# Kernel tuning notes

Measured on AMD Instinct MI355X. Metric: run time of the kernel, lower is better.

## Reference

```python
import jax, jax.numpy as jnp
from jax import lax
import numpy as np

DN = ('NCHW', 'OIHW', 'NCHW')
EPS = 1e-5


def conv3(x, w, b=None):
    # 3x3 conv, stride 1, padding 1 (SAME)
    y = lax.conv_general_dilated(x, w, (1, 1), 'SAME', dimension_numbers=DN)
    return y if b is None else y + b[None, :, None, None]


def bn_relu(x, gamma, beta):
    # training-mode BatchNorm2d (batch statistics over N,H,W) + ReLU
    m = jnp.mean(x, axis=(0, 2, 3), keepdims=True)
    v = jnp.var(x, axis=(0, 2, 3), keepdims=True)
    y = (x - m) * lax.rsqrt(v + EPS)
    y = y * gamma[None, :, None, None] + beta[None, :, None, None]
    return jax.nn.relu(y)


def _w(key, o, i):
    # torch init: normal(0, sqrt(2/(k*k*out)))
    std = np.sqrt(2.0 / (3 * 3 * o))
    return jax.random.normal(key, (o, i, 3, 3), dtype=jnp.float32) * std


def setup_inputs() -> dict:
    key = jax.random.key(0)
    ks = jax.random.split(key, 16)
    C = 256
    Ch = C // 2
    B, H, W = 4, 160, 160
    d = {}
    d['fpn_fea'] = jax.random.normal(ks[0], (B, C, H, W), dtype=jnp.float32)
    # sc_smooth_layer: conv(C->C)+BN+ReLU, conv(C->C/2)+BN+ReLU (no conv bias)
    d['w_sc1'] = _w(ks[1], C, C); d['g_sc1'] = jnp.ones((C,)); d['b_sc1'] = jnp.zeros((C,))
    d['w_sc2'] = _w(ks[2], Ch, C); d['g_sc2'] = jnp.ones((Ch,)); d['b_sc2'] = jnp.zeros((Ch,))
    # shrink / centroid heads: plain conv(C/2 -> 1) with bias
    d['w_shrink'] = _w(ks[3], 1, Ch); d['bias_shrink'] = jnp.zeros((1,))
    d['w_cent'] = _w(ks[4], 1, Ch); d['bias_cent'] = jnp.zeros((1,))
    # param_head
    d['w_p1'] = _w(ks[5], C, C); d['g_p1'] = jnp.ones((C,)); d['b_p1'] = jnp.zeros((C,))
    d['w_p2'] = _w(ks[6], Ch, C); d['g_p2'] = jnp.ones((Ch,)); d['b_p2'] = jnp.zeros((Ch,))
    d['w_p3'] = _w(ks[7], 2, Ch); d['bias_p3'] = jnp.zeros((2,))
    # shift_head
    d['w_s1'] = _w(ks[8], C, C); d['g_s1'] = jnp.ones((C,)); d['b_s1'] = jnp.zeros((C,))
    d['w_s2'] = _w(ks[9], Ch, C); d['g_s2'] = jnp.ones((Ch,)); d['b_s2'] = jnp.zeros((Ch,))
    d['w_s3'] = _w(ks[10], 8, Ch); d['bias_s3'] = jnp.zeros((8,))
    return d


def reference(fpn_fea, w_sc1, g_sc1, b_sc1, w_sc2, g_sc2, b_sc2,
              w_shrink, bias_shrink, w_cent, bias_cent,
              w_p1, g_p1, b_p1, w_p2, g_p2, b_p2, w_p3, bias_p3,
              w_s1, g_s1, b_s1, w_s2, g_s2, b_s2, w_s3, bias_s3):
    smooth = bn_relu(conv3(fpn_fea, w_sc1), g_sc1, b_sc1)
    smooth = bn_relu(conv3(smooth, w_sc2), g_sc2, b_sc2)
    shrink = conv3(smooth, w_shrink, bias_shrink)      # [B,1,H,W]
    centroid = conv3(smooth, w_cent, bias_cent)        # [B,1,H,W]
    p = bn_relu(conv3(fpn_fea, w_p1), g_p1, b_p1)
    p = bn_relu(conv3(p, w_p2), g_p2, b_p2)
    param = conv3(p, w_p3, bias_p3)                    # [B,2,H,W]
    s = bn_relu(conv3(fpn_fea, w_s1), g_s1, b_s1)
    s = bn_relu(conv3(s, w_s2), g_s2, b_s2)
    shift = conv3(s, w_s3, bias_s3)                    # [B,8,H,W]
    return (shrink, centroid, param, shift)
```

## Files before the change

kernel.cpp:

```cpp
#include <hip/hip_runtime.h>

typedef short bf16x8 __attribute__((ext_vector_type(8)));
typedef float f32x4 __attribute__((ext_vector_type(4)));

__device__ __forceinline__ float bf2f(unsigned short u) {
    union { unsigned int i; float f; } c; c.i = ((unsigned int)u) << 16; return c.f;
}
__device__ __forceinline__ unsigned short f2bf(float f) {
    union { float f; unsigned int i; } c; c.f = f;
    unsigned int u = c.i;
    u += 0x7fffu + ((u >> 16) & 1u);
    return (unsigned short)(u >> 16);
}

__device__ __forceinline__ void gload_lds16(const unsigned short* g, unsigned short* l) {
    __builtin_amdgcn_global_load_lds(
        (const __attribute__((address_space(1))) void*)g,
        (__attribute__((address_space(3))) void*)l, 16, 0, 0);
}


__device__ __forceinline__ void zero_border_one(unsigned short* buf, int C, int idx) {
    int CV = C >> 3;
    int cv = idx % CV; int t = idx / CV;
    int p = t % 644;   int n = t / 644;
    int h, w;
    if (p < 162)      { h = 0;   w = p; }
    else if (p < 324) { h = 161; w = p - 162; }
    else { int q = p - 324; h = 1 + (q >> 1); w = (q & 1) ? 161 : 0; }
    uint4 z = make_uint4(0u, 0u, 0u, 0u);
    *(uint4*)(buf + ((size_t)((n * 162 + h) * 162) + w) * C + cv * 8) = z;
}

__device__ __forceinline__ void do_zero(unsigned short* xpad,
                                        unsigned short* buf1, size_t s1,
                                        unsigned short* buf2, size_t s2, int nbr, int idx) {
    if (idx < 82432) { zero_border_one(xpad, 256, idx); return; }
    idx -= 82432;
    int nb1 = nbr * 82432;
    if (idx < nb1) { zero_border_one(buf1 + (size_t)(idx / 82432) * s1, 256, idx % 82432); return; }
    idx -= nb1;
    int nb2 = nbr * 41216;
    if (idx < nb2) { zero_border_one(buf2 + (size_t)(idx / 41216) * s2, 128, idx % 41216); }
}

__device__ __forceinline__ void do_transpose(const float* __restrict__ x,
                                             unsigned short* __restrict__ xpad, int idx) {
    int w = idx % 160; int t = idx / 160;
    int cv = t % 32;   t /= 32;
    int h = t % 160;   int n = t / 160;
    const float* src = x + (((size_t)(n * 256 + cv * 8) * 160 + h) * 160 + w);
    unsigned short us[8];
#pragma unroll
    for (int k = 0; k < 8; ++k) us[k] = f2bf(src[(size_t)k * 25600]);
    uint4 o;
    o.x = (unsigned int)us[0] | ((unsigned int)us[1] << 16);
    o.y = (unsigned int)us[2] | ((unsigned int)us[3] << 16);
    o.z = (unsigned int)us[4] | ((unsigned int)us[5] << 16);
    o.w = (unsigned int)us[6] | ((unsigned int)us[7] << 16);
    *(uint4*)(xpad + ((size_t)((n * 162 + h + 1) * 162) + (w + 1)) * 256 + cv * 8) = o;
}

__device__ __forceinline__ void do_pack(const float* s0, const float* s1, const float* s2,
                                        const float* s3, const float* s4, const float* s5,
                                        unsigned short* w1p, unsigned short* w2p, int idx) {
    int t = idx / 294912, r = idx - t * 294912;
    const float* src; unsigned short* dst; int coBase;
    if (t < 6) {
        int br = t >> 1;
        src = (br == 0) ? s0 : (br == 1) ? s1 : s2;
        coBase = (t & 1) * 128;
        dst = w1p + (size_t)t * 294912;
    } else {
        int br = t - 6;
        src = (br == 0) ? s3 : (br == 1) ? s4 : s5;
        coBase = 0;
        dst = w2p + (size_t)br * 294912;
    }
    int tap, ci, o;
    if (r < 262144) {
        int tp = r >> 16, rem = r & 65535;
        int q = rem >> 13, r2 = rem & 8191;
        int e = r2 & 7, gco = r2 >> 3;
        int co = gco & 127, g = gco >> 7;
        tap = tp * 2 + (g >> 2);
        ci = q * 32 + (g & 3) * 8 + e;
        o = coBase + co;
    } else {
        int rem = r - 262144;
        int q = rem >> 12, r2 = rem & 4095;
        int e = r2 & 7, gco = r2 >> 3;
        int co = gco & 127, g = gco >> 7;
        tap = 8;
        ci = q * 32 + g * 8 + e;
        o = coBase + co;
    }
    dst[r] = f2bf(src[((size_t)(o * 256 + ci)) * 9 + tap]);
}

__global__ void prep(const float* __restrict__ fpn, unsigned short* __restrict__ xpad,
                     unsigned short* __restrict__ buf1, size_t s1,
                     unsigned short* __restrict__ buf2, size_t s2, int nbr,
                     int zb, int zcount,
                     const float* w10, const float* w11, const float* w12,
                     const float* w20, const float* w21, const float* w22,
                     unsigned short* __restrict__ w1p, unsigned short* __restrict__ w2p) {
    int bid = blockIdx.x;
    if (bid < zb) {
        int idx = bid * 256 + threadIdx.x;
        if (idx < zcount) do_zero(xpad, buf1, s1, buf2, s2, nbr, idx);
        return;
    }
    bid -= zb;
    if (bid < 12800) { do_transpose(fpn, xpad, bid * 256 + threadIdx.x); return; }
    bid -= 12800;
    do_pack(w10, w11, w12, w20, w21, w22, w1p, w2p, bid * 256 + threadIdx.x);
}

template<int COT, int BPB>
__global__ __launch_bounds__(256, 2) void conv3x3_mfma(
        const unsigned short* __restrict__ xpad0, size_t xstride,
        const unsigned short* __restrict__ wpk0, size_t wstride,
        unsigned short* __restrict__ ypad0, size_t ystride,
        float* __restrict__ stats, int sstride) {
    __shared__ __align__(16) unsigned short As[16384];
    __shared__ __align__(16) unsigned short Bs[12288];

    const int br = blockIdx.x / BPB;
    int bid = blockIdx.x % BPB;
    const unsigned short* xpad = xpad0 + (size_t)br * xstride;
    const unsigned short* wpk  = wpk0 + (size_t)br * wstride;
    unsigned short* ypad       = ypad0 + (size_t)br * ystride;
    float* sum   = stats + (size_t)br * sstride;
    float* sumsq = sum + 256;

    const int tid = threadIdx.x;
    const int wv = tid >> 6, lane = tid & 63;
    const int quad = lane >> 4, l15 = lane & 15;
    const int wco = wv >> 1, wsp = wv & 1;

    const int wt = bid % 5;
    const int ht = (bid / 5) % 20;
    const int n = (bid / 100) % 4;
    const int tile = bid / 400;
    const int co0 = tile * 128;
    const int h0 = ht * 8, w0 = wt * 32;

    const unsigned short* wtile = wpk + (size_t)tile * 294912;

    int boff[6];
#pragma unroll
    for (int r = 0; r < 6; ++r) {
        int slot = r * 256 + tid;
        int g = slot / 384, p = slot - g * 384;
        if (p > 339) p = 339;
        int prow = p / 34, pcol = p - prow * 34;
        boff[r] = ((n * 162 + h0 + prow) * 162 + (w0 + pcol)) * 256 + g * 8;
    }

    int p0[8];
#pragma unroll
    for (int j = 0; j < 8; ++j) {
        int sp = wsp * 128 + j * 16 + l15;
        p0[j] = (sp >> 5) * 34 + (sp & 31);
    }

    f32x4 acc[4][8];
#pragma unroll
    for (int i = 0; i < 4; ++i)
#pragma unroll
        for (int j = 0; j < 8; ++j) acc[i][j] = (f32x4){0.f, 0.f, 0.f, 0.f};

    for (int q = 0; q < 8; ++q) {
#pragma unroll
        for (int w = 0; w < 3; ++w) {
            __syncthreads();
            if (w == 0) {
                const unsigned short* bq = xpad + q * 32;
#pragma unroll
                for (int r = 0; r < 6; ++r)
                    gload_lds16(bq + boff[r], (unsigned short*)Bs + (r * 256 + tid) * 8);
            }
            if (w < 2) {
#pragma unroll
                for (int h = 0; h < 2; ++h) {
                    const unsigned short* asrc = wtile + (w * 2 + h) * 65536 + q * 8192 + tid * 8;
#pragma unroll
                    for (int c = 0; c < 4; ++c)
                        gload_lds16(asrc + c * 2048,
                                    (unsigned short*)As + h * 8192 + c * 2048 + tid * 8);
                }
            } else {
                const unsigned short* asrc = wtile + 262144 + q * 4096 + tid * 8;
#pragma unroll
                for (int c = 0; c < 2; ++c)
                    gload_lds16(asrc + c * 2048, (unsigned short*)As + c * 2048 + tid * 8);
            }
            __syncthreads();

#pragma unroll
            for (int t = 0; t < 4; ++t) {
                if (w == 2 && t >= 1) continue;
                const int TAP = (w < 2) ? (w * 4 + t) : 8;
                const int dh = TAP / 3, dw = TAP % 3;
                const int toff = dh * 34 + dw;
                const int g0 = (w < 2) ? ((t & 1) * 4 + quad) : quad;
                const unsigned short* Ab = As + ((w < 2) ? (t >> 1) * 8192 : 0);
                bf16x8 a[4];
#pragma unroll
                for (int i = 0; i < 4; ++i)
                    a[i] = *(const bf16x8*)(Ab + (size_t)(g0 * 128 + wco * 64 + i * 16 + l15) * 8);
#pragma unroll
                for (int jh = 0; jh < 2; ++jh) {
                    bf16x8 b[4];
#pragma unroll
                    for (int j = 0; j < 4; ++j)
                        b[j] = *(const bf16x8*)(Bs + (size_t)(quad * 384 + p0[jh * 4 + j] + toff) * 8);
#pragma unroll
                    for (int i = 0; i < 4; ++i)
#pragma unroll
                        for (int j = 0; j < 4; ++j)
                            acc[i][jh * 4 + j] = __builtin_amdgcn_mfma_f32_16x16x32_bf16(
                                a[i], b[j], acc[i][jh * 4 + j], 0, 0, 0);
                }
            }
        }
    }

#pragma unroll
    for (int i = 0; i < 4; ++i) {
        const int co_l = wco * 64 + i * 16 + quad * 4;
#pragma unroll
        for (int j = 0; j < 8; ++j) {
            const int sp = wsp * 128 + j * 16 + l15;
            const int jh = sp >> 5, jw = sp & 31;
            f32x4 v = acc[i][j];
            ushort4 pk;
            pk.x = f2bf(v[0]); pk.y = f2bf(v[1]); pk.z = f2bf(v[2]); pk.w = f2bf(v[3]);
            *(ushort4*)(ypad + ((size_t)((n * 162 + h0 + jh + 1) * 162) + (w0 + jw + 1)) * COT
                        + co0 + co_l) = pk;
        }
#pragma unroll
        for (int r = 0; r < 4; ++r) {
            float s1 = 0.f, s2 = 0.f;
#pragma unroll
            for (int j = 0; j < 8; ++j) { float v = acc[i][j][r]; s1 += v; s2 += v * v; }
#pragma unroll
            for (int m = 1; m < 16; m <<= 1) {
                s1 += __shfl_xor(s1, m, 64);
                s2 += __shfl_xor(s2, m, 64);
            }
            if (l15 == 0) {
                atomicAdd(&sum[co0 + co_l + r], s1);
                atomicAdd(&sumsq[co0 + co_l + r], s2);
            }
        }
    }
}

template<int C, int BPB>
__global__ void bn_apply(unsigned short* __restrict__ buf0, size_t bstride,
                         const float* __restrict__ stats, int sstride,
                         const float* g0, const float* g1, const float* g2,
                         const float* be0, const float* be1, const float* be2) {
    const int br = blockIdx.x / BPB;
    unsigned short* buf = buf0 + (size_t)br * bstride;
    const float* sum = stats + (size_t)br * sstride;
    const float* sumsq = sum + 256;
    const float* gamma = (br == 0) ? g0 : (br == 1) ? g1 : g2;
    const float* beta  = (br == 0) ? be0 : (br == 1) ? be1 : be2;

    __shared__ float s_sc[C], s_sh[C];
    if (threadIdx.x < C) {
        int c = threadIdx.x;
        const float inv = 1.0f / 102400.0f;
        float m = sum[c] * inv;
        float v = sumsq[c] * inv - m * m;
        float sc = gamma[c] * rsqrtf(v + 1e-5f);
        s_sc[c] = sc;
        s_sh[c] = beta[c] - m * sc;
    }
    __syncthreads();

    constexpr int CV = C / 8;
    int idx = (blockIdx.x % BPB) * 256 + threadIdx.x;
    int cv = idx % CV; int pos = idx / CV;
    int w = pos % 160; int h = (pos / 160) % 160; int n = pos / 25600;
    unsigned short* p = buf + ((size_t)((n * 162 + h + 1) * 162) + (w + 1)) * C + cv * 8;
    uint4 v = *(const uint4*)p;
    unsigned int ua[4] = {v.x, v.y, v.z, v.w};
    unsigned int ob[4];
#pragma unroll
    for (int j = 0; j < 4; ++j) {
        int c = cv * 8 + j * 2;
        float f0 = bf2f((unsigned short)(ua[j] & 0xffffu)) * s_sc[c] + s_sh[c];
        float f1 = bf2f((unsigned short)(ua[j] >> 16)) * s_sc[c + 1] + s_sh[c + 1];
        f0 = fmaxf(f0, 0.f); f1 = fmaxf(f1, 0.f);
        ob[j] = (unsigned int)f2bf(f0) | ((unsigned int)f2bf(f1) << 16);
    }
    uint4 o = make_uint4(ob[0], ob[1], ob[2], ob[3]);
    *(uint4*)p = o;
}

template<int CO>
__global__ __launch_bounds__(256) void head_conv(const unsigned short* __restrict__ z,
                                                 const float* __restrict__ w,
                                                 const float* __restrict__ bias,
                                                 float* __restrict__ out) {
    __shared__ float s_w[CO * 9 * 128];
    __shared__ __align__(16) unsigned short s_z[1536 * 8];
    for (int t = threadIdx.x; t < CO * 9 * 128; t += 256) {
        int ci = t % 128; int r = t / 128;
        int tap = r % 9;  int o = r / 9;
        s_w[t] = w[((size_t)(o * 128 + ci)) * 9 + tap];
    }

    const int bid = blockIdx.x;
    const int wt = bid % 5, ht = (bid / 5) % 20, n = bid / 100;
    const int h0 = ht * 8, w0 = wt * 32;
    const int tid = threadIdx.x;

    int zoff[6];
#pragma unroll
    for (int r = 0; r < 6; ++r) {
        int slot = r * 256 + tid;
        if (slot > 1359) slot = 1359;
        int c8 = slot / 340, pos = slot - c8 * 340;
        int prow = pos / 34, pcol = pos - prow * 34;
        zoff[r] = ((n * 162 + h0 + prow) * 162 + (w0 + pcol)) * 128 + c8 * 8;
    }
    const int prow_t = tid >> 5, pcol_t = tid & 31;

    float acc[CO];
#pragma unroll
    for (int o = 0; o < CO; ++o) acc[o] = bias[o];

    for (int ph = 0; ph < 4; ++ph) {
        __syncthreads();
#pragma unroll
        for (int r = 0; r < 6; ++r)
            gload_lds16(z + zoff[r] + ph * 32, (unsigned short*)s_z + (r * 256 + tid) * 8);
        __syncthreads();

#pragma unroll
        for (int dh = 0; dh < 3; ++dh)
#pragma unroll
            for (int dw = 0; dw < 3; ++dw) {
                const int tap = dh * 3 + dw;
                const int pos = (prow_t + dh) * 34 + pcol_t + dw;
#pragma unroll
                for (int c8 = 0; c8 < 4; ++c8) {
                    uint4 v = *(const uint4*)(s_z + (size_t)(c8 * 340 + pos) * 8);
                    unsigned int ua[4] = {v.x, v.y, v.z, v.w};
                    float xv[8];
#pragma unroll
                    for (int j = 0; j < 4; ++j) {
                        xv[2 * j]     = bf2f((unsigned short)(ua[j] & 0xffffu));
                        xv[2 * j + 1] = bf2f((unsigned short)(ua[j] >> 16));
                    }
#pragma unroll
                    for (int o = 0; o < CO; ++o) {
                        const float* wp = &s_w[(o * 9 + tap) * 128 + ph * 32 + c8 * 8];
                        float4 w0v = *(const float4*)wp;
                        float4 w1v = *(const float4*)(wp + 4);
                        acc[o] = fmaf(xv[0], w0v.x, acc[o]);
                        acc[o] = fmaf(xv[1], w0v.y, acc[o]);
                        acc[o] = fmaf(xv[2], w0v.z, acc[o]);
                        acc[o] = fmaf(xv[3], w0v.w, acc[o]);
                        acc[o] = fmaf(xv[4], w1v.x, acc[o]);
                        acc[o] = fmaf(xv[5], w1v.y, acc[o]);
                        acc[o] = fmaf(xv[6], w1v.z, acc[o]);
                        acc[o] = fmaf(xv[7], w1v.w, acc[o]);
                    }
                }
            }
    }
    const int pw = w0 + pcol_t, phh = h0 + prow_t;
#pragma unroll
    for (int o = 0; o < CO; ++o)
        out[((size_t)(n * CO + o)) * 25600 + phh * 160 + pw] = acc[o];
}

__global__ __launch_bounds__(256) void head_conv_dual(const unsigned short* __restrict__ z,
                                                      const float* __restrict__ w1, const float* __restrict__ b1,
                                                      const float* __restrict__ w2, const float* __restrict__ b2,
                                                      float* __restrict__ out1, float* __restrict__ out2) {
    __shared__ float s_w[2 * 9 * 128];
    __shared__ __align__(16) unsigned short s_z[1536 * 8];
    for (int t = threadIdx.x; t < 2 * 9 * 128; t += 256) {
        int ci = t % 128; int r = t / 128;
        int tap = r % 9;  int which = r / 9;
        const float* src = which ? w2 : w1;
        s_w[t] = src[(size_t)ci * 9 + tap];
    }

    const int bid = blockIdx.x;
    const int wt = bid % 5, ht = (bid / 5) % 20, n = bid / 100;
    const int h0 = ht * 8, w0 = wt * 32;
    const int tid = threadIdx.x;

    int zoff[6];
#pragma unroll
    for (int r = 0; r < 6; ++r) {
        int slot = r * 256 + tid;
        if (slot > 1359) slot = 1359;
        int c8 = slot / 340, pos = slot - c8 * 340;
        int prow = pos / 34, pcol = pos - prow * 34;
        zoff[r] = ((n * 162 + h0 + prow) * 162 + (w0 + pcol)) * 128 + c8 * 8;
    }
    const int prow_t = tid >> 5, pcol_t = tid & 31;

    float a1 = b1[0], a2 = b2[0];

    for (int ph = 0; ph < 4; ++ph) {
        __syncthreads();
#pragma unroll
        for (int r = 0; r < 6; ++r)
            gload_lds16(z + zoff[r] + ph * 32, (unsigned short*)s_z + (r * 256 + tid) * 8);
        __syncthreads();

#pragma unroll
        for (int dh = 0; dh < 3; ++dh)
#pragma unroll
            for (int dw = 0; dw < 3; ++dw) {
                const int tap = dh * 3 + dw;
                const int pos = (prow_t + dh) * 34 + pcol_t + dw;
#pragma unroll
                for (int c8 = 0; c8 < 4; ++c8) {
                    uint4 v = *(const uint4*)(s_z + (size_t)(c8 * 340 + pos) * 8);
                    unsigned int ua[4] = {v.x, v.y, v.z, v.w};
                    float xv[8];
#pragma unroll
                    for (int j = 0; j < 4; ++j) {
                        xv[2 * j]     = bf2f((unsigned short)(ua[j] & 0xffffu));
                        xv[2 * j + 1] = bf2f((unsigned short)(ua[j] >> 16));
                    }
                    const float* wp1 = &s_w[tap * 128 + ph * 32 + c8 * 8];
                    const float* wp2 = &s_w[1152 + tap * 128 + ph * 32 + c8 * 8];
#pragma unroll
                    for (int e = 0; e < 8; ++e) {
                        a1 = fmaf(xv[e], wp1[e], a1);
                        a2 = fmaf(xv[e], wp2[e], a2);
                    }
                }
            }
    }
    const int pw = w0 + pcol_t, phh = h0 + prow_t;
    out1[(size_t)n * 25600 + phh * 160 + pw] = a1;
    out2[(size_t)n * 25600 + phh * 160 + pw] = a2;
}

extern "C" void kernel_launch(void* const* d_in, const int* in_sizes, int n_in,
                              void* d_out, int out_size, void* d_ws, size_t ws_size,
                              hipStream_t stream) {
    const float* fpn = (const float*)d_in[0];
    const float* W1[3] = {(const float*)d_in[1],  (const float*)d_in[11], (const float*)d_in[19]};
    const float* G1[3] = {(const float*)d_in[2],  (const float*)d_in[12], (const float*)d_in[20]};
    const float* B1[3] = {(const float*)d_in[3],  (const float*)d_in[13], (const float*)d_in[21]};
    const float* W2[3] = {(const float*)d_in[4],  (const float*)d_in[14], (const float*)d_in[22]};
    const float* G2[3] = {(const float*)d_in[5],  (const float*)d_in[15], (const float*)d_in[23]};
    const float* B2[3] = {(const float*)d_in[6],  (const float*)d_in[16], (const float*)d_in[24]};
    const float* w_shrink = (const float*)d_in[7];  const float* b_shrink = (const float*)d_in[8];
    const float* w_cent   = (const float*)d_in[9];  const float* b_cent   = (const float*)d_in[10];
    const float* w_p3     = (const float*)d_in[17]; const float* b_p3     = (const float*)d_in[18];
    const float* w_s3     = (const float*)d_in[25]; const float* b_s3     = (const float*)d_in[26];
    float* out = (float*)d_out;

    const size_t S1 = (size_t)4 * 162 * 162 * 256;
    const size_t S2 = (size_t)4 * 162 * 162 * 128;
    const size_t need_fused = S1 * 2 * 4  + S2 * 2 * 3
                              + (size_t)9 * 294912 * 2 + 6 * 512 * 4;

    char* ws = (char*)d_ws;
    size_t off = 0;
    unsigned short* xpad = (unsigned short*)(ws + off); off += S1 * 2;
    const int NBR = (ws_size >= need_fused) ? 3 : 1;
    unsigned short* buf1 = (unsigned short*)(ws + off); off += S1 * 2 * NBR;
    unsigned short* buf2 = (unsigned short*)(ws + off); off += S2 * 2 * NBR;
    unsigned short* w1p  = (unsigned short*)(ws + off); off += (size_t)6 * 294912 * 2;
    unsigned short* w2p  = (unsigned short*)(ws + off); off += (size_t)3 * 294912 * 2;
    float* stats         = (float*)(ws + off);          off += (size_t)6 * 512 * 4;

    hipMemsetAsync(stats, 0, 6 * 512 * 4, stream);
    {
        int zcount = 82432 * (1 + NBR) + 41216 * NBR;
        int zb = (zcount + 255) / 256;
        prep<<<zb + 12800 + 10368, 256, 0, stream>>>(
            fpn, xpad, buf1, S1, buf2, S2, NBR, zb, zcount,
            W1[0], W1[1], W1[2], W2[0], W2[1], W2[2], w1p, w2p);
    }

    if (NBR == 3) {
        conv3x3_mfma<256, 800><<<2400, 256, 0, stream>>>(
            xpad, 0, w1p, (size_t)2 * 294912, buf1, S1, stats, 1024);
        bn_apply<256, 12800><<<38400, 256, 0, stream>>>(
            buf1, S1, stats, 1024, G1[0], G1[1], G1[2], B1[0], B1[1], B1[2]);
        conv3x3_mfma<128, 400><<<1200, 256, 0, stream>>>(
            buf1, S1, w2p, (size_t)294912, buf2, S2, stats + 512, 1024);
        bn_apply<128, 6400><<<19200, 256, 0, stream>>>(
            buf2, S2, stats + 512, 1024, G2[0], G2[1], G2[2], B2[0], B2[1], B2[2]);
        head_conv_dual<<<400, 256, 0, stream>>>(buf2, w_shrink, b_shrink, w_cent, b_cent,
                                                out, out + 102400);
        head_conv<2><<<400, 256, 0, stream>>>(buf2 + S2, w_p3, b_p3, out + 204800);
        head_conv<8><<<400, 256, 0, stream>>>(buf2 + 2 * S2, w_s3, b_s3, out + 409600);
    } else {
        for (int br = 0; br < 3; ++br) {
            conv3x3_mfma<256, 800><<<800, 256, 0, stream>>>(
                xpad, 0, w1p + (size_t)br * 2 * 294912, 0, buf1, 0, stats + br * 1024, 0);
            bn_apply<256, 12800><<<12800, 256, 0, stream>>>(
                buf1, 0, stats + br * 1024, 0, G1[br], G1[br], G1[br], B1[br], B1[br], B1[br]);
            conv3x3_mfma<128, 400><<<400, 256, 0, stream>>>(
                buf1, 0, w2p + (size_t)br * 294912, 0, buf2, 0, stats + 512 + br * 1024, 0);
            bn_apply<128, 6400><<<6400, 256, 0, stream>>>(
                buf2, 0, stats + 512 + br * 1024, 0, G2[br], G2[br], G2[br], B2[br], B2[br], B2[br]);
            if (br == 0) {
                head_conv_dual<<<400, 256, 0, stream>>>(buf2, w_shrink, b_shrink, w_cent, b_cent,
                                                        out, out + 102400);
            } else if (br == 1) {
                head_conv<2><<<400, 256, 0, stream>>>(buf2, w_p3, b_p3, out + 204800);
            } else {
                head_conv<8><<<400, 256, 0, stream>>>(buf2, w_s3, b_s3, out + 409600);
            }
        }
    }
}
```

Before: 1.196 ms.

## Shrink conv LDS footprint by staging weights per tap pair and packing input tile

The 3x3 conv kernel now loads one 2-tap weight slab per stage instead of 4 taps. This takes the K-loop from 3 to 5 stages per channel chunk and halves the weight LDS buffer. The input tile's per-group stride is packed from 384 to 340 rows, removing padding slots. The aim is a smaller shared memory footprint, allowing more resident blocks per CU. The cost is more __syncthreads barriers and load/compute phases per iteration.

```diff
diff --git a/kernel.cpp b/kernel.cpp
--- a/kernel.cpp
+++ b/kernel.cpp
@@ -123,8 +123,8 @@
         const unsigned short* __restrict__ wpk0, size_t wstride,
         unsigned short* __restrict__ ypad0, size_t ystride,
         float* __restrict__ stats, int sstride) {
-    __shared__ __align__(16) unsigned short As[16384];
-    __shared__ __align__(16) unsigned short Bs[12288];
+    __shared__ __align__(16) unsigned short As[8192];
+    __shared__ __align__(16) unsigned short Bs[10880];
 
     const int br = blockIdx.x / BPB;
     int bid = blockIdx.x % BPB;
@@ -152,8 +152,8 @@
 #pragma unroll
     for (int r = 0; r < 6; ++r) {
         int slot = r * 256 + tid;
-        int g = slot / 384, p = slot - g * 384;
-        if (p > 339) p = 339;
+        if (slot > 1359) slot = 1359;
+        int g = slot / 340, p = slot - g * 340;
         int prow = p / 34, pcol = p - prow * 34;
         boff[r] = ((n * 162 + h0 + prow) * 162 + (w0 + pcol)) * 256 + g * 8;
     }
@@ -173,23 +173,21 @@
 
     for (int q = 0; q < 8; ++q) {
 #pragma unroll
-        for (int w = 0; w < 3; ++w) {
+        for (int w = 0; w < 5; ++w) {
             __syncthreads();
             if (w == 0) {
-                const unsigned short* bq = xpad + q * 32;
-#pragma unroll
-                for (int r = 0; r < 6; ++r)
-                    gload_lds16(bq + boff[r], (unsigned short*)Bs + (r * 256 + tid) * 8);
-            }
-            if (w < 2) {
-#pragma unroll
-                for (int h = 0; h < 2; ++h) {
-                    const unsigned short* asrc = wtile + (w * 2 + h) * 65536 + q * 8192 + tid * 8;
-#pragma unroll
-                    for (int c = 0; c < 4; ++c)
-                        gload_lds16(asrc + c * 2048,
-                                    (unsigned short*)As + h * 8192 + c * 2048 + tid * 8);
-                }
+                const unsigned short* bqp = xpad + q * 32;
+#pragma unroll
+                for (int r = 0; r < 5; ++r)
+                    gload_lds16(bqp + boff[r], (unsigned short*)Bs + (r * 256 + tid) * 8);
+                if (tid < 80)
+                    gload_lds16(bqp + boff[5], (unsigned short*)Bs + (1280 + tid) * 8);
+            }
+            if (w < 4) {
+                const unsigned short* asrc = wtile + w * 65536 + q * 8192 + tid * 8;
+#pragma unroll
+                for (int c = 0; c < 4; ++c)
+                    gload_lds16(asrc + c * 2048, (unsigned short*)As + c * 2048 + tid * 8);
             } else {
                 const unsigned short* asrc = wtile + 262144 + q * 4096 + tid * 8;
 #pragma unroll
@@ -199,23 +197,22 @@
             __syncthreads();
 
 #pragma unroll
-            for (int t = 0; t < 4; ++t) {
-                if (w == 2 && t >= 1) continue;
-                const int TAP = (w < 2) ? (w * 4 + t) : 8;
+            for (int ts = 0; ts < 2; ++ts) {
+                if (w == 4 && ts == 1) continue;
+                const int TAP = (w < 4) ? (w * 2 + ts) : 8;
                 const int dh = TAP / 3, dw = TAP % 3;
                 const int toff = dh * 34 + dw;
-                const int g0 = (w < 2) ? ((t & 1) * 4 + quad) : quad;
-                const unsigned short* Ab = As + ((w < 2) ? (t >> 1) * 8192 : 0);
+                const int g0 = (w < 4 ? ts * 4 : 0) + quad;
                 bf16x8 a[4];
 #pragma unroll
                 for (int i = 0; i < 4; ++i)
-                    a[i] = *(const bf16x8*)(Ab + (size_t)(g0 * 128 + wco * 64 + i * 16 + l15) * 8);
+                    a[i] = *(const bf16x8*)(As + (size_t)(g0 * 128 + wco * 64 + i * 16 + l15) * 8);
 #pragma unroll
                 for (int jh = 0; jh < 2; ++jh) {
                     bf16x8 b[4];
 #pragma unroll
                     for (int j = 0; j < 4; ++j)
-                        b[j] = *(const bf16x8*)(Bs + (size_t)(quad * 384 + p0[jh * 4 + j] + toff) * 8);
+                        b[j] = *(const bf16x8*)(Bs + (size_t)(quad * 340 + p0[jh * 4 + j] + toff) * 8);
 #pragma unroll
                     for (int i = 0; i < 4; ++i)
 #pragma unroll
@@ -229,7 +226,7 @@
 
 #pragma unroll
     for (int i = 0; i < 4; ++i) {
-        const int co_l = wco * 64 + i * 16 + quad * 4;
+        const int co_e = wco * 64 + i * 16 + quad * 4;
 #pragma unroll
         for (int j = 0; j < 8; ++j) {
             const int sp = wsp * 128 + j * 16 + l15;
@@ -238,7 +235,7 @@
             ushort4 pk;
             pk.x = f2bf(v[0]); pk.y = f2bf(v[1]); pk.z = f2bf(v[2]); pk.w = f2bf(v[3]);
             *(ushort4*)(ypad + ((size_t)((n * 162 + h0 + jh + 1) * 162) + (w0 + jw + 1)) * COT
-                        + co0 + co_l) = pk;
+                        + co0 + co_e) = pk;
         }
 #pragma unroll
         for (int r = 0; r < 4; ++r) {
@@ -251,8 +248,8 @@
                 s2 += __shfl_xor(s2, m, 64);
             }
             if (l15 == 0) {
-                atomicAdd(&sum[co0 + co_l + r], s1);
-                atomicAdd(&sumsq[co0 + co_l + r], s2);
+                atomicAdd(&sum[co0 + co_e + r], s1);
+                atomicAdd(&sumsq[co0 + co_e + r], s2);
             }
         }
     }
```

New measurement: 1.181 ms. About the same (-1.2%).

## Fuse second BN+ReLU into a single all-branch head conv kernel

Applied to the files above, without the earlier changes.

Replaces the second-stage bn_apply pass and three separate head-conv launches with one heads_all kernel. It computes the BN scale and shift from the stats, then applies normalize and ReLU on the fly while loading tiles into LDS, masking padded border positions to zero. This removes a full read-modify-write pass over the 128-channel activations and several launches. The stats memset is also folded into the prep kernel. The per-element BN math in the head inner loop is repeated for each tap, which adds ALU work. The fallback head kernels are simplified to direct global loads.

```diff
diff --git a/kernel.cpp b/kernel.cpp
--- a/kernel.cpp
+++ b/kernel.cpp
@@ -101,11 +101,16 @@
 __global__ void prep(const float* __restrict__ fpn, unsigned short* __restrict__ xpad,
                      unsigned short* __restrict__ buf1, size_t s1,
                      unsigned short* __restrict__ buf2, size_t s2, int nbr,
-                     int zb, int zcount,
+                     int zb, int zcount, float* __restrict__ stats,
                      const float* w10, const float* w11, const float* w12,
                      const float* w20, const float* w21, const float* w22,
                      unsigned short* __restrict__ w1p, unsigned short* __restrict__ w2p) {
     int bid = blockIdx.x;
+    if (bid < 3) {
+        ((float4*)stats)[bid * 256 + threadIdx.x] = make_float4(0.f, 0.f, 0.f, 0.f);
+        return;
+    }
+    bid -= 3;
     if (bid < zb) {
         int idx = bid * 256 + threadIdx.x;
         if (idx < zcount) do_zero(xpad, buf1, s1, buf2, s2, nbr, idx);
@@ -302,83 +307,186 @@
     *(uint4*)p = o;
 }
 
+__global__ __launch_bounds__(256) void heads_all(
+        const unsigned short* __restrict__ zb, size_t zstride,
+        const float* __restrict__ stats2, int sstride,
+        const float* g20, const float* g21, const float* g22,
+        const float* be20, const float* be21, const float* be22,
+        const float* w_sh, const float* bi_sh, const float* w_ce, const float* bi_ce,
+        const float* w_p3, const float* bi_p3, const float* w_s3, const float* bi_s3,
+        float* __restrict__ out) {
+    const int br = blockIdx.x / 400;
+    const int bid = blockIdx.x % 400;
+    const unsigned short* z = zb + (size_t)br * zstride;
+    const float* sum   = stats2 + (size_t)br * sstride;
+    const float* sumsq = sum + 256;
+    const float* gamma = (br == 0) ? g20 : (br == 1) ? g21 : g22;
+    const float* beta  = (br == 0) ? be20 : (br == 1) ? be21 : be22;
+
+    __shared__ float s_sc[128], s_sh[128];
+    __shared__ float s_w[8 * 9 * 128];
+    __shared__ __align__(16) unsigned short s_z[1536 * 8];
+
+    const int tid = threadIdx.x;
+    if (tid < 128) {
+        const float inv = 1.0f / 102400.0f;
+        float m = sum[tid] * inv;
+        float v = sumsq[tid] * inv - m * m;
+        float sc = gamma[tid] * rsqrtf(v + 1e-5f);
+        s_sc[tid] = sc;
+        s_sh[tid] = beta[tid] - m * sc;
+    }
+    if (br == 0) {
+        for (int t = tid; t < 2 * 1152; t += 256) {
+            int ci = t % 128; int r = t / 128;
+            int tap = r % 9;  int which = r / 9;
+            const float* src = which ? w_ce : w_sh;
+            s_w[t] = src[(size_t)ci * 9 + tap];
+        }
+    } else {
+        const float* wsrc = (br == 1) ? w_p3 : w_s3;
+        const int nco = (br == 1) ? 2 : 8;
+        for (int t = tid; t < nco * 1152; t += 256) {
+            int ci = t % 128; int r = t / 128;
+            int tap = r % 9;  int o = r / 9;
+            s_w[t] = wsrc[((size_t)(o * 128 + ci)) * 9 + tap];
+        }
+    }
+
+    const int wt = bid % 5, ht = (bid / 5) % 20, n = bid / 100;
+    const int h0 = ht * 8, w0 = wt * 32;
+
+    int zoff[6];
+#pragma unroll
+    for (int r = 0; r < 6; ++r) {
+        int slot = r * 256 + tid;
+        if (slot > 1359) slot = 1359;
+        int c8 = slot / 340, pos = slot - c8 * 340;
+        int prow = pos / 34, pcol = pos - prow * 34;
+        zoff[r] = ((n * 162 + h0 + prow) * 162 + (w0 + pcol)) * 128 + c8 * 8;
+    }
+    const int prow_t = tid >> 5, pcol_t = tid & 31;
+
+    float acc[8];
+#pragma unroll
+    for (int o = 0; o < 8; ++o) acc[o] = 0.f;
+
+    for (int ph = 0; ph < 4; ++ph) {
+        __syncthreads();
+#pragma unroll
+        for (int r = 0; r < 6; ++r)
+            gload_lds16(z + zoff[r] + ph * 32, (unsigned short*)s_z + (r * 256 + tid) * 8);
+        __syncthreads();
+
+#pragma unroll
+        for (int dh = 0; dh < 3; ++dh)
+#pragma unroll
+            for (int dw = 0; dw < 3; ++dw) {
+                const int tap = dh * 3 + dw;
+                const int pos = (prow_t + dh) * 34 + pcol_t + dw;
+                const int hh = h0 + prow_t + dh, ww = w0 + pcol_t + dw;
+                const bool edge = (hh == 0) | (hh == 161) | (ww == 0) | (ww == 161);
+#pragma unroll
+                for (int c8 = 0; c8 < 4; ++c8) {
+                    uint4 v = *(const uint4*)(s_z + (size_t)(c8 * 340 + pos) * 8);
+                    unsigned int ua[4] = {v.x, v.y, v.z, v.w};
+                    float zv[8];
+#pragma unroll
+                    for (int j = 0; j < 4; ++j) {
+                        int c = ph * 32 + c8 * 8 + 2 * j;
+                        float x0 = bf2f((unsigned short)(ua[j] & 0xffffu));
+                        float x1 = bf2f((unsigned short)(ua[j] >> 16));
+                        float y0 = fmaxf(x0 * s_sc[c] + s_sh[c], 0.f);
+                        float y1 = fmaxf(x1 * s_sc[c + 1] + s_sh[c + 1], 0.f);
+                        zv[2 * j]     = edge ? 0.f : y0;
+                        zv[2 * j + 1] = edge ? 0.f : y1;
+                    }
+                    if (br == 0) {
+                        const float* wp1 = &s_w[tap * 128 + ph * 32 + c8 * 8];
+                        const float* wp2 = &s_w[1152 + tap * 128 + ph * 32 + c8 * 8];
+#pragma unroll
+                        for (int e = 0; e < 8; ++e) {
+                            acc[0] = fmaf(zv[e], wp1[e], acc[0]);
+                            acc[1] = fmaf(zv[e], wp2[e], acc[1]);
+                        }
+                    } else if (br == 1) {
+#pragma unroll
+                        for (int o = 0; o < 2; ++o) {
+                            const float* wp = &s_w[(o * 9 + tap) * 128 + ph * 32 + c8 * 8];
+#pragma unroll
+                            for (int e = 0; e < 8; ++e)
+                                acc[o] = fmaf(zv[e], wp[e], acc[o]);
+                        }
+                    } else {
+#pragma unroll
+                        for (int o = 0; o < 8; ++o) {
+                            const float* wp = &s_w[(o * 9 + tap) * 128 + ph * 32 + c8 * 8];
+#pragma unroll
+                            for (int e = 0; e < 8; ++e)
+                                acc[o] = fmaf(zv[e], wp[e], acc[o]);
+                        }
+                    }
+                }
+            }
+    }
+    const int pw = w0 + pcol_t, phh = h0 + prow_t;
+    if (br == 0) {
+        out[(size_t)n * 25600 + phh * 160 + pw] = acc[0] + bi_sh[0];
+        out[102400 + (size_t)n * 25600 + phh * 160 + pw] = acc[1] + bi_ce[0];
+    } else if (br == 1) {
+#pragma unroll
+        for (int o = 0; o < 2; ++o)
+            out[204800 + ((size_t)(n * 2 + o)) * 25600 + phh * 160 + pw] = acc[o] + bi_p3[o];
+    } else {
+#pragma unroll
+        for (int o = 0; o < 8; ++o)
+            out[409600 + ((size_t)(n * 8 + o)) * 25600 + phh * 160 + pw] = acc[o] + bi_s3[o];
+    }
+}
+
 template<int CO>
 __global__ __launch_bounds__(256) void head_conv(const unsigned short* __restrict__ z,
                                                  const float* __restrict__ w,
                                                  const float* __restrict__ bias,
                                                  float* __restrict__ out) {
     __shared__ float s_w[CO * 9 * 128];
-    __shared__ __align__(16) unsigned short s_z[1536 * 8];
     for (int t = threadIdx.x; t < CO * 9 * 128; t += 256) {
         int ci = t % 128; int r = t / 128;
         int tap = r % 9;  int o = r / 9;
         s_w[t] = w[((size_t)(o * 128 + ci)) * 9 + tap];
     }
-
-    const int bid = blockIdx.x;
-    const int wt = bid % 5, ht = (bid / 5) % 20, n = bid / 100;
-    const int h0 = ht * 8, w0 = wt * 32;
-    const int tid = threadIdx.x;
-
-    int zoff[6];
-#pragma unroll
-    for (int r = 0; r < 6; ++r) {
-        int slot = r * 256 + tid;
-        if (slot > 1359) slot = 1359;
-        int c8 = slot / 340, pos = slot - c8 * 340;
-        int prow = pos / 34, pcol = pos - prow * 34;
-        zoff[r] = ((n * 162 + h0 + prow) * 162 + (w0 + pcol)) * 128 + c8 * 8;
-    }
-    const int prow_t = tid >> 5, pcol_t = tid & 31;
-
+    __syncthreads();
+    const int pos = blockIdx.x * 256 + threadIdx.x;
+    const int pw = pos % 160, ph = (pos / 160) % 160, pn = pos / 25600;
     float acc[CO];
 #pragma unroll
     for (int o = 0; o < CO; ++o) acc[o] = bias[o];
-
-    for (int ph = 0; ph < 4; ++ph) {
-        __syncthreads();
-#pragma unroll
-        for (int r = 0; r < 6; ++r)
-            gload_lds16(z + zoff[r] + ph * 32, (unsigned short*)s_z + (r * 256 + tid) * 8);
-        __syncthreads();
-
-#pragma unroll
-        for (int dh = 0; dh < 3; ++dh)
-#pragma unroll
-            for (int dw = 0; dw < 3; ++dw) {
-                const int tap = dh * 3 + dw;
-                const int pos = (prow_t + dh) * 34 + pcol_t + dw;
-#pragma unroll
-                for (int c8 = 0; c8 < 4; ++c8) {
-                    uint4 v = *(const uint4*)(s_z + (size_t)(c8 * 340 + pos) * 8);
-                    unsigned int ua[4] = {v.x, v.y, v.z, v.w};
-                    float xv[8];
-#pragma unroll
-                    for (int j = 0; j < 4; ++j) {
-                        xv[2 * j]     = bf2f((unsigned short)(ua[j] & 0xffffu));
-                        xv[2 * j + 1] = bf2f((unsigned short)(ua[j] >> 16));
-                    }
-#pragma unroll
-                    for (int o = 0; o < CO; ++o) {
-                        const float* wp = &s_w[(o * 9 + tap) * 128 + ph * 32 + c8 * 8];
-                        float4 w0v = *(const float4*)wp;
-                        float4 w1v = *(const float4*)(wp + 4);
-                        acc[o] = fmaf(xv[0], w0v.x, acc[o]);
-                        acc[o] = fmaf(xv[1], w0v.y, acc[o]);
-                        acc[o] = fmaf(xv[2], w0v.z, acc[o]);
-                        acc[o] = fmaf(xv[3], w0v.w, acc[o]);
-                        acc[o] = fmaf(xv[4], w1v.x, acc[o]);
-                        acc[o] = fmaf(xv[5], w1v.y, acc[o]);
-                        acc[o] = fmaf(xv[6], w1v.z, acc[o]);
-                        acc[o] = fmaf(xv[7], w1v.w, acc[o]);
-                    }
+#pragma unroll
+    for (int dh = 0; dh < 3; ++dh)
+#pragma unroll
+        for (int dw = 0; dw < 3; ++dw) {
+            const int tap = dh * 3 + dw;
+            const unsigned short* zp = z + ((size_t)((pn * 162 + ph + dh) * 162) + (pw + dw)) * 128;
+            for (int c8 = 0; c8 < 16; ++c8) {
+                uint4 v = *(const uint4*)(zp + c8 * 8);
+                unsigned int ua[4] = {v.x, v.y, v.z, v.w};
+                float xv[8];
+#pragma unroll
+                for (int j = 0; j < 4; ++j) {
+                    xv[2 * j]     = bf2f((unsigned short)(ua[j] & 0xffffu));
+                    xv[2 * j + 1] = bf2f((unsigned short)(ua[j] >> 16));
                 }
-            }
-    }
-    const int pw = w0 + pcol_t, phh = h0 + prow_t;
+#pragma unroll
+                for (int o = 0; o < CO; ++o) {
+                    const float* wp = &s_w[(o * 9 + tap) * 128 + c8 * 8];
+#pragma unroll
+                    for (int e = 0; e < 8; ++e) acc[o] = fmaf(xv[e], wp[e], acc[o]);
+                }
+            }
+        }
 #pragma unroll
     for (int o = 0; o < CO; ++o)
-        out[((size_t)(n * CO + o)) * 25600 + phh * 160 + pw] = acc[o];
+        out[((size_t)(pn * CO + o)) * 25600 + ph * 160 + pw] = acc[o];
 }
 
 __global__ __launch_bounds__(256) void head_conv_dual(const unsigned short* __restrict__ z,
@@ -386,68 +494,42 @@
                                                       const float* __restrict__ w2, const float* __restrict__ b2,
                                                       float* __restrict__ out1, float* __restrict__ out2) {
     __shared__ float s_w[2 * 9 * 128];
-    __shared__ __align__(16) unsigned short s_z[1536 * 8];
     for (int t = threadIdx.x; t < 2 * 9 * 128; t += 256) {
         int ci = t % 128; int r = t / 128;
         int tap = r % 9;  int which = r / 9;
         const float* src = which ? w2 : w1;
         s_w[t] = src[(size_t)ci * 9 + tap];
     }
-
-    const int bid = blockIdx.x;
-    const int wt = bid % 5, ht = (bid / 5) % 20, n = bid / 100;
-    const int h0 = ht * 8, w0 = wt * 32;
-    const int tid = threadIdx.x;
-
-    int zoff[6];
-#pragma unroll
-    for (int r = 0; r < 6; ++r) {
-        int slot = r * 256 + tid;
-        if (slot > 1359) slot = 1359;
-        int c8 = slot / 340, pos = slot - c8 * 340;
-        int prow = pos / 34, pcol = pos - prow * 34;
-        zoff[r] = ((n * 162 + h0 + prow) * 162 + (w0 + pcol)) * 128 + c8 * 8;
-    }
-    const int prow_t = tid >> 5, pcol_t = tid & 31;
-
+    __syncthreads();
+    const int pos = blockIdx.x * 256 + threadIdx.x;
+    const int pw = pos % 160, ph = (pos / 160) % 160, pn = pos / 25600;
     float a1 = b1[0], a2 = b2[0];
-
-    for (int ph = 0; ph < 4; ++ph) {
-        __syncthreads();
-#pragma unroll
-        for (int r = 0; r < 6; ++r)
-            gload_lds16(z + zoff[r] + ph * 32, (unsigned short*)s_z + (r * 256 + tid) * 8);
-        __syncthreads();
-
-#pragma unroll
-        for (int dh = 0; dh < 3; ++dh)
-#pragma unroll
-            for (int dw = 0; dw < 3; ++dw) {
-                const int tap = dh * 3 + dw;
-                const int pos = (prow_t + dh) * 34 + pcol_t + dw;
-#pragma unroll
-                for (int c8 = 0; c8 < 4; ++c8) {
-                    uint4 v = *(const uint4*)(s_z + (size_t)(c8 * 340 + pos) * 8);
-                    unsigned int ua[4] = {v.x, v.y, v.z, v.w};
-                    float xv[8];
-#pragma unroll
-                    for (int j = 0; j < 4; ++j) {
-                        xv[2 * j]     = bf2f((unsigned short)(ua[j] & 0xffffu));
-                        xv[2 * j + 1] = bf2f((unsigned short)(ua[j] >> 16));
-                    }
-                    const float* wp1 = &s_w[tap * 128 + ph * 32 + c8 * 8];
-                    const float* wp2 = &s_w[1152 + tap * 128 + ph * 32 + c8 * 8];
-#pragma unroll
-                    for (int e = 0; e < 8; ++e) {
-                        a1 = fmaf(xv[e], wp1[e], a1);
-                        a2 = fmaf(xv[e], wp2[e], a2);
-                    }
+#pragma unroll
+    for (int dh = 0; dh < 3; ++dh)
+#pragma unroll
+        for (int dw = 0; dw < 3; ++dw) {
+            const int tap = dh * 3 + dw;
+            const unsigned short* zp = z + ((size_t)((pn * 162 + ph + dh) * 162) + (pw + dw)) * 128;
+            for (int c8 = 0; c8 < 16; ++c8) {
+                uint4 v = *(const uint4*)(zp + c8 * 8);
+                unsigned int ua[4] = {v.x, v.y, v.z, v.w};
+                float xv[8];
+#pragma unroll
+                for (int j = 0; j < 4; ++j) {
+                    xv[2 * j]     = bf2f((unsigned short)(ua[j] & 0xffffu));
+                    xv[2 * j + 1] = bf2f((unsigned short)(ua[j] >> 16));
                 }
-            }
-    }
-    const int pw = w0 + pcol_t, phh = h0 + prow_t;
-    out1[(size_t)n * 25600 + phh * 160 + pw] = a1;
-    out2[(size_t)n * 25600 + phh * 160 + pw] = a2;
+                const float* wp1 = &s_w[tap * 128 + c8 * 8];
+                const float* wp2 = &s_w[1152 + tap * 128 + c8 * 8];
+#pragma unroll
+                for (int e = 0; e < 8; ++e) {
+                    a1 = fmaf(xv[e], wp1[e], a1);
+                    a2 = fmaf(xv[e], wp2[e], a2);
+                }
+            }
+        }
+    out1[(size_t)pn * 25600 + ph * 160 + pw] = a1;
+    out2[(size_t)pn * 25600 + ph * 160 + pw] = a2;
 }
 
 extern "C" void kernel_launch(void* const* d_in, const int* in_sizes, int n_in,
@@ -468,7 +550,7 @@
 
     const size_t S1 = (size_t)4 * 162 * 162 * 256;
     const size_t S2 = (size_t)4 * 162 * 162 * 128;
-    const size_t need_fused = S1 * 2 * 4  + S2 * 2 * 3
+    const size_t need_fused = S1 * 2 * 4 + S2 * 2 * 3
                               + (size_t)9 * 294912 * 2 + 6 * 512 * 4;
 
     char* ws = (char*)d_ws;
@@ -481,12 +563,11 @@
     unsigned short* w2p  = (unsigned short*)(ws + off); off += (size_t)3 * 294912 * 2;
     float* stats         = (float*)(ws + off);          off += (size_t)6 * 512 * 4;
 
-    hipMemsetAsync(stats, 0, 6 * 512 * 4, stream);
     {
         int zcount = 82432 * (1 + NBR) + 41216 * NBR;
         int zb = (zcount + 255) / 256;
-        prep<<<zb + 12800 + 10368, 256, 0, stream>>>(
-            fpn, xpad, buf1, S1, buf2, S2, NBR, zb, zcount,
+        prep<<<3 + zb + 12800 + 10368, 256, 0, stream>>>(
+            fpn, xpad, buf1, S1, buf2, S2, NBR, zb, zcount, stats,
             W1[0], W1[1], W1[2], W2[0], W2[1], W2[2], w1p, w2p);
     }
 
@@ -497,12 +578,10 @@
             buf1, S1, stats, 1024, G1[0], G1[1], G1[2], B1[0], B1[1], B1[2]);
         conv3x3_mfma<128, 400><<<1200, 256, 0, stream>>>(
             buf1, S1, w2p, (size_t)294912, buf2, S2, stats + 512, 1024);
-        bn_apply<128, 6400><<<19200, 256, 0, stream>>>(
-            buf2, S2, stats + 512, 1024, G2[0], G2[1], G2[2], B2[0], B2[1], B2[2]);
-        head_conv_dual<<<400, 256, 0, stream>>>(buf2, w_shrink, b_shrink, w_cent, b_cent,
-                                                out, out + 102400);
-        head_conv<2><<<400, 256, 0, stream>>>(buf2 + S2, w_p3, b_p3, out + 204800);
-        head_conv<8><<<400, 256, 0, stream>>>(buf2 + 2 * S2, w_s3, b_s3, out + 409600);
+        heads_all<<<1200, 256, 0, stream>>>(
+            buf2, S2, stats + 512, 1024,
+            G2[0], G2[1], G2[2], B2[0], B2[1], B2[2],
+            w_shrink, b_shrink, w_cent, b_cent, w_p3, b_p3, w_s3, b_s3, out);
     } else {
         for (int br = 0; br < 3; ++br) {
             conv3x3_mfma<256, 800><<<800, 256, 0, stream>>>(
```

New measurement: 1.147 ms. -4.1%, faster.
